# Kernel tuning notes

Measured on AMD Instinct MI355X. Metric: run time of the kernel, lower is better.

## Reference

```python
import jax, jax.numpy as jnp
import numpy as np

EMBED = 768
HEADS = 12
HEAD_DIM = EMBED // HEADS
FFN = 4 * EMBED
EPS = 1e-5


def setup_inputs() -> dict:
    key = jax.random.key(0)
    ks = jax.random.split(key, 12)
    s = 0.02
    inp = {
        'x': jax.random.normal(ks[0], (1, 4096, EMBED), dtype=jnp.float32),
        'Wq': jax.random.normal(ks[1], (EMBED, EMBED), dtype=jnp.float32) * s,
        'bq': jnp.zeros((EMBED,), jnp.float32),
        'Wk': jax.random.normal(ks[2], (EMBED, EMBED), dtype=jnp.float32) * s,
        'bk': jnp.zeros((EMBED,), jnp.float32),
        'Wv': jax.random.normal(ks[3], (EMBED, EMBED), dtype=jnp.float32) * s,
        'bv': jnp.zeros((EMBED,), jnp.float32),
        'Wo': jax.random.normal(ks[4], (EMBED, EMBED), dtype=jnp.float32) * s,
        'bo': jnp.zeros((EMBED,), jnp.float32),
        'ln1_g': jnp.ones((EMBED,), jnp.float32),
        'ln1_b': jnp.zeros((EMBED,), jnp.float32),
        'W1': jax.random.normal(ks[5], (EMBED, FFN), dtype=jnp.float32) * s,
        'b1': jnp.zeros((FFN,), jnp.float32),
        'W2': jax.random.normal(ks[6], (FFN, EMBED), dtype=jnp.float32) * s,
        'b2': jnp.zeros((EMBED,), jnp.float32),
        'ln2_g': jnp.ones((EMBED,), jnp.float32),
        'ln2_b': jnp.zeros((EMBED,), jnp.float32),
    }
    return inp


def _layernorm(x, g, b):
    mu = jnp.mean(x, axis=-1, keepdims=True)
    var = jnp.mean(jnp.square(x - mu), axis=-1, keepdims=True)
    return (x - mu) * jax.lax.rsqrt(var + EPS) * g + b


def reference(x, Wq, bq, Wk, bk, Wv, bv, Wo, bo, ln1_g, ln1_b, W1, b1, W2, b2, ln2_g, ln2_b):
    B, S, D = x.shape
    # QKV projections -> [B, H, S, d]
    def split_heads(t):
        return t.reshape(B, S, HEADS, HEAD_DIM).transpose(0, 2, 1, 3)
    q = split_heads(x @ Wq + bq)
    k = split_heads(x @ Wk + bk)
    v = split_heads(x @ Wv + bv)
    scores = jnp.einsum('bhqd,bhkd->bhqk', q, k) / np.sqrt(HEAD_DIM).astype(np.float32)
    attn = jax.nn.softmax(scores, axis=-1)
    ctx = jnp.einsum('bhqk,bhkd->bhqd', attn, v)
    ctx = ctx.transpose(0, 2, 1, 3).reshape(B, S, D)
    attn_out = ctx @ Wo + bo
    h = _layernorm(x + attn_out, ln1_g, ln1_b)
    ffn = jax.nn.gelu(h @ W1 + b1, approximate=False) @ W2 + b2
    return _layernorm(h + ffn, ln2_g, ln2_b)
```

## Files before the change

kernel.cpp:

```cpp
#include <hip/hip_runtime.h>
#include <hip/hip_bf16.h>

typedef __attribute__((ext_vector_type(8))) short s16x8;
typedef __attribute__((ext_vector_type(4))) short s16x4;
typedef __attribute__((ext_vector_type(4))) int   i32x4;
typedef __attribute__((ext_vector_type(4))) float f32x4;
typedef __attribute__((ext_vector_type(8))) __bf16 bf16x8;
typedef __attribute__((ext_vector_type(4))) __bf16 bf16x4;

__device__ __forceinline__ short f2bf(float f) {
  unsigned u = __builtin_bit_cast(unsigned, f);
  u = (u + 0x7FFFu + ((u >> 16) & 1u)) >> 16;
  return (short)u;
}
__device__ __forceinline__ float bf2f(short s) {
  unsigned u = ((unsigned)(unsigned short)s) << 16;
  return __builtin_bit_cast(float, u);
}
__device__ __forceinline__ f32x4 mfma16(s16x8 a, s16x8 b, f32x4 c) {
  return __builtin_amdgcn_mfma_f32_16x16x32_bf16(
      __builtin_bit_cast(bf16x8, a), __builtin_bit_cast(bf16x8, b), c, 0, 0, 0);
}
__device__ __forceinline__ void gload16(const void* g, void* l) {
  __builtin_amdgcn_global_load_lds(
      (const __attribute__((address_space(1))) void*)g,
      (__attribute__((address_space(3))) void*)l, 16, 0, 0);
}

__global__ __launch_bounds__(256) void prep_kernel(
    const float* __restrict__ x, short* __restrict__ xb,
    const float* __restrict__ bq, const float* __restrict__ bk,
    const float* __restrict__ bv, float* __restrict__ bqkv,
    const float* __restrict__ Wq, const float* __restrict__ Wk,
    const float* __restrict__ Wv, const float* __restrict__ Wo,
    const float* __restrict__ W1, const float* __restrict__ W2,
    short* __restrict__ wqkv_t, short* __restrict__ wo_t,
    short* __restrict__ w1_t, short* __restrict__ w2_t) {
  __shared__ float t[32][33];
  const int b = blockIdx.x, tid = threadIdx.x;
  if (b < 1536) {
    int i = b * 256 + tid;
    float4 v0 = ((const float4*)x)[i * 2];
    float4 v1 = ((const float4*)x)[i * 2 + 1];
    s16x8 o;
    o[0] = f2bf(v0.x); o[1] = f2bf(v0.y); o[2] = f2bf(v0.z); o[3] = f2bf(v0.w);
    o[4] = f2bf(v1.x); o[5] = f2bf(v1.y); o[6] = f2bf(v1.z); o[7] = f2bf(v1.w);
    *(s16x8*)&xb[i * 8] = o;
    return;
  }
  if (b < 1545) {
    int i = (b - 1536) * 256 + tid;
    if (i < 2304) bqkv[i] = i < 768 ? bq[i] : (i < 1536 ? bk[i - 768] : bv[i - 1536]);
    return;
  }
  const float* src; short* dst; int K, N, bx, by;
  if (b < 3849) {
    int t4 = b - 1545, wi = t4 / 576, r = t4 % 576;
    bx = r % 24; by = r / 24; K = 768; N = 768;
    src = wi == 0 ? Wq : wi == 1 ? Wk : wi == 2 ? Wv : Wo;
    dst = wi == 0 ? wqkv_t : wi == 1 ? wqkv_t + 768 * 768
        : wi == 2 ? wqkv_t + 2 * 768 * 768 : wo_t;
  } else if (b < 6153) {
    int r = b - 3849; bx = r % 96; by = r / 96; K = 768; N = 3072; src = W1; dst = w1_t;
  } else {
    int r = b - 6153; bx = r % 24; by = r / 24; K = 3072; N = 768; src = W2; dst = w2_t;
  }
  int n0 = bx * 32, k0 = by * 32;
  int tx = tid & 31, ty = tid >> 5;
#pragma unroll
  for (int r = 0; r < 4; ++r) t[ty + r * 8][tx] = src[(long)(k0 + ty + r * 8) * N + n0 + tx];
  __syncthreads();
#pragma unroll
  for (int r = 0; r < 4; ++r)
    dst[(long)(n0 + ty + r * 8) * K + k0 + tx] = f2bf(t[tx][ty + r * 8]);
}

template <int OUT_MODE>
__global__ __launch_bounds__(256) void gemm_kernel(const short* __restrict__ A,
                                                   const short* __restrict__ Bt,
                                                   const float* __restrict__ bias,
                                                   void* __restrict__ Cout,
                                                   short* __restrict__ vtout,
                                                   int M, int N, int Kfull, int Ksub) {
  __shared__ short As[3][64 * 64];
  __shared__ short Bs[3][64 * 64];
  const int tid = threadIdx.x;
  const int wave = tid >> 6, lane = tid & 63;
  const int lr = lane & 15, lg = lane >> 4;
  const int wm = wave >> 1, wn = wave & 1;
  const int bm = blockIdx.x, bn = blockIdx.y;
  const long koff = (long)blockIdx.z * Ksub;

  f32x4 acc[4][4] = {};

  const short* Ab = A + (long)bm * 128 * Kfull + koff;
  const short* Bb = Bt + (long)bn * 128 * Kfull + koff;

  int sj[2], sr[2], skc[2];
#pragma unroll
  for (int rnd = 0; rnd < 2; ++rnd) {
    int c = tid + rnd * 256;
    int j = c >> 3, c7 = c & 7;
    int u = c7 ^ (j & 7);
    sj[rnd] = c;
    sr[rnd] = j + ((u >> 2) << 6);
    skc[rnd] = (u & 3) * 8;
  }

  auto STAGE = [&](int buf, int k0) {
#pragma unroll
    for (int rnd = 0; rnd < 2; ++rnd) {
      gload16(Ab + (long)sr[rnd] * Kfull + k0 + skc[rnd], &As[buf][sj[rnd] * 8]);
      gload16(Bb + (long)sr[rnd] * Kfull + k0 + skc[rnd], &Bs[buf][sj[rnd] * 8]);
    }
  };
  auto COMPUTE = [&](int buf) {
    s16x8 af[4], bfr[4];
#pragma unroll
    for (int m = 0; m < 4; ++m) {
      int j = m * 16 + lr;
      int c7 = ((wm << 2) | lg) ^ (lr & 7);
      af[m] = *(const s16x8*)&As[buf][j * 64 + c7 * 8];
    }
#pragma unroll
    for (int n = 0; n < 4; ++n) {
      int j = n * 16 + lr;
      int c7 = ((wn << 2) | lg) ^ (lr & 7);
      bfr[n] = *(const s16x8*)&Bs[buf][j * 64 + c7 * 8];
    }
#pragma unroll
    for (int m = 0; m < 4; ++m)
#pragma unroll
      for (int n = 0; n < 4; ++n)
        acc[m][n] = mfma16(af[m], bfr[n], acc[m][n]);
  };

  const int nt = Ksub >> 5;
  STAGE(0, 0);
  STAGE(1, 32);
  int cur = 0;
  for (int t = 0; t < nt - 2; ++t) {
    int nb = cur + 2; if (nb >= 3) nb -= 3;
    STAGE(nb, (t + 2) * 32);
    asm volatile("s_waitcnt vmcnt(8)" ::: "memory");
    __builtin_amdgcn_s_barrier();
    __builtin_amdgcn_sched_barrier(0);
    COMPUTE(cur);
    __builtin_amdgcn_s_barrier();
    cur = (cur == 2) ? 0 : cur + 1;
  }
  asm volatile("s_waitcnt vmcnt(4)" ::: "memory");
  __builtin_amdgcn_s_barrier();
  __builtin_amdgcn_sched_barrier(0);
  COMPUTE(cur);
  __builtin_amdgcn_s_barrier();
  cur = (cur == 2) ? 0 : cur + 1;
  asm volatile("s_waitcnt vmcnt(0)" ::: "memory");
  __builtin_amdgcn_s_barrier();
  __builtin_amdgcn_sched_barrier(0);
  COMPUTE(cur);

  const int gr0 = bm * 128 + wm * 64 + lg * 4;
  const int gc0 = bn * 128 + wn * 64 + lr;
  if (OUT_MODE == 0 && vtout != nullptr && bn >= 12) {
#pragma unroll
    for (int n = 0; n < 4; ++n) {
      int col = gc0 + n * 16;
      float bb = bias[col];
#pragma unroll
      for (int m = 0; m < 4; ++m) {
        s16x4 pk;
#pragma unroll
        for (int j = 0; j < 4; ++j) pk[j] = f2bf(acc[m][n][j] + bb);
        *(s16x4*)&vtout[(long)(col - 1536) * 4096 + gr0 + m * 16] = pk;
      }
    }
    return;
  }
  float* outF = (float*)Cout + (long)blockIdx.z * M * N;
#pragma unroll
  for (int n = 0; n < 4; ++n) {
    int col = gc0 + n * 16;
    float bb = (blockIdx.z == 0) ? bias[col] : 0.f;
#pragma unroll
    for (int m = 0; m < 4; ++m) {
#pragma unroll
      for (int j = 0; j < 4; ++j) {
        int row = gr0 + m * 16 + j;
        float v = acc[m][n][j] + bb;
        if (OUT_MODE == 2) v = 0.5f * v * (1.0f + erff(v * 0.70710678118f));
        if (OUT_MODE == 1) outF[(long)row * N + col] = v;
        else ((short*)Cout)[(long)row * N + col] = f2bf(v);
      }
    }
  }
}

__global__ __launch_bounds__(256) void flash_kernel(const short* __restrict__ qkv,
                                                    const short* __restrict__ vt,
                                                    short* __restrict__ Opart,
                                                    float* __restrict__ Lpart) {
  __shared__ short Kt[2][64 * 64];
  __shared__ short Vs[2][64 * 64];
  __shared__ short Ps[128 * 72];
  const int tid = threadIdx.x;
  const int wave = tid >> 6, lane = tid & 63;
  const int lr = lane & 15, lg = lane >> 4;
  const int lb = blockIdx.x + 32 * blockIdx.y + 384 * blockIdx.z;
  const int nlb = (lb & 7) * 96 + (lb >> 3);
  const int qb = nlb & 31;
  const int h = (nlb >> 5) % 12;
  const int sp = nlb / 384;
  const int qc = h * 64;
  const int hc = 768 + h * 64;
  const int vr = h * 64;
  const float QSCALE = 0.125f * 1.44269504088896f;
  const int sbase = sp * 2048;

  auto STAGE = [&](int buf, int it) {
    const int s0 = sbase + it * 64;
#pragma unroll
    for (int i = 0; i < 2; ++i) {
      int c = tid + i * 256, row = c >> 3, ch = (c & 7) ^ (row & 7);
      gload16(&qkv[(long)(s0 + row) * 2304 + hc + ch * 8], &Kt[buf][c * 8]);
      gload16(&vt[(long)(vr + row) * 4096 + s0 + ch * 8], &Vs[buf][c * 8]);
    }
  };

  STAGE(0, 0);

#pragma unroll
  for (int i = 0; i < 4; ++i) {
    int c = tid + i * 256;
    int row = c >> 3, cq = (c & 7) * 8;
    *(i32x4*)&Ps[row * 72 + cq] =
        *(const i32x4*)&qkv[(long)(qb * 128 + row) * 2304 + qc + cq];
  }
  asm volatile("s_waitcnt vmcnt(0) lgkmcnt(0)" ::: "memory");
  __builtin_amdgcn_s_barrier();
  __builtin_amdgcn_sched_barrier(0);

  s16x8 qf[2][2];
#pragma unroll
  for (int m = 0; m < 2; ++m)
#pragma unroll
    for (int ks = 0; ks < 2; ++ks) {
      int row = wave * 32 + m * 16 + lr;
      s16x8 v = *(const s16x8*)&Ps[row * 72 + ks * 32 + lg * 8];
#pragma unroll
      for (int e = 0; e < 8; ++e) {
        __bf16 b = (__bf16)(bf2f(v[e]) * QSCALE);
        v[e] = (short)__builtin_bit_cast(unsigned short, b);
      }
      qf[m][ks] = v;
    }

  float l_part[2] = {0.f, 0.f};
  f32x4 oacc[2][4] = {};

  int cur = 0;
  for (int it = 0; it < 32; ++it) {
    if (it < 31) STAGE(cur ^ 1, it + 1);

    f32x4 sacc[2][4] = {};
#pragma unroll
    for (int ks = 0; ks < 2; ++ks) {
      s16x8 kf[4];
#pragma unroll
      for (int n = 0; n < 4; ++n) {
        int row = n * 16 + lr;
        int chk = (ks * 4 + lg) ^ (lr & 7);
        kf[n] = *(const s16x8*)&Kt[cur][row * 64 + chk * 8];
      }
      __builtin_amdgcn_s_setprio(1);
#pragma unroll
      for (int m = 0; m < 2; ++m)
#pragma unroll
        for (int n = 0; n < 4; ++n)
          sacc[m][n] = mfma16(kf[n], qf[m][ks], sacc[m][n]);
      __builtin_amdgcn_s_setprio(0);
    }
#pragma unroll
    for (int m = 0; m < 2; ++m) {
      const int prow = wave * 32 + m * 16 + lr;
      float rs = 0.f;
#pragma unroll
      for (int n = 0; n < 4; ++n) {
        float p0 = __builtin_amdgcn_exp2f(sacc[m][n][0]);
        float p1 = __builtin_amdgcn_exp2f(sacc[m][n][1]);
        float p2 = __builtin_amdgcn_exp2f(sacc[m][n][2]);
        float p3 = __builtin_amdgcn_exp2f(sacc[m][n][3]);
        rs += (p0 + p1) + (p2 + p3);
        bf16x4 pk;
        pk[0] = (__bf16)p0; pk[1] = (__bf16)p1;
        pk[2] = (__bf16)p2; pk[3] = (__bf16)p3;
        *(bf16x4*)&Ps[prow * 72 + n * 16 + lg * 4] = pk;
      }
      l_part[m] += rs;
    }
#pragma unroll
    for (int ks = 0; ks < 2; ++ks) {
      s16x8 pf[2], vf[4];
#pragma unroll
      for (int m = 0; m < 2; ++m) {
        int row = wave * 32 + m * 16 + lr;
        pf[m] = *(const s16x8*)&Ps[row * 72 + ks * 32 + lg * 8];
      }
#pragma unroll
      for (int n = 0; n < 4; ++n) {
        int row = n * 16 + lr;
        int chk = (ks * 4 + lg) ^ (lr & 7);
        vf[n] = *(const s16x8*)&Vs[cur][row * 64 + chk * 8];
      }
      __builtin_amdgcn_s_setprio(1);
#pragma unroll
      for (int m = 0; m < 2; ++m)
#pragma unroll
        for (int n = 0; n < 4; ++n)
          oacc[m][n] = mfma16(pf[m], vf[n], oacc[m][n]);
      __builtin_amdgcn_s_setprio(0);
    }
    if (it < 31) {
      asm volatile("s_waitcnt vmcnt(0)" ::: "memory");
      __builtin_amdgcn_s_barrier();
      __builtin_amdgcn_sched_barrier(0);
      cur ^= 1;
    }
  }

  const long pbase = ((long)(h * 32 + qb) * 2 + sp) * 128;
#pragma unroll
  for (int m = 0; m < 2; ++m) {
    float l = l_part[m];
    l += __shfl_xor(l, 16);
    l += __shfl_xor(l, 32);
    if (lane < 16) Lpart[pbase + wave * 32 + m * 16 + lr] = l;
  }
#pragma unroll
  for (int m = 0; m < 2; ++m)
#pragma unroll
    for (int n = 0; n < 4; ++n)
#pragma unroll
      for (int j = 0; j < 4; ++j) {
        int row = wave * 32 + m * 16 + lg * 4 + j;
        Opart[(pbase + row) * 64 + n * 16 + lr] = f2bf(oacc[m][n][j]);
      }
}

__global__ __launch_bounds__(256) void combine_kernel(const short* __restrict__ Opart,
                                                      const float* __restrict__ Lpart,
                                                      short* __restrict__ ctx) {
  const int row = blockIdx.x;
  const int col = blockIdx.y * 256 + threadIdx.x;
  const int h = col >> 6, c = col & 63;
  const int qb = row >> 7, r = row & 127;
  const long p0 = ((long)(h * 32 + qb) * 2) * 128 + r;
  const long p1 = p0 + 128;
  float l = Lpart[p0] + Lpart[p1];
  float o = bf2f(Opart[p0 * 64 + c]) + bf2f(Opart[p1 * 64 + c]);
  ctx[(long)row * 768 + col] = f2bf(o / l);
}

template <int AF, int OF>
__global__ __launch_bounds__(256) void ln_kernel(const void* __restrict__ a_,
                                                 const float* __restrict__ b,
                                                 const float* __restrict__ c,
                                                 const float* __restrict__ g,
                                                 const float* __restrict__ be,
                                                 void* __restrict__ out_) {
  const int row = blockIdx.x;
  const int tid = threadIdx.x;
  const long base = (long)row * 768;
  float v[3];
  float s1 = 0.f, s2 = 0.f;
#pragma unroll
  for (int kk = 0; kk < 3; ++kk) {
    int i = tid + kk * 256;
    float av = AF ? ((const float*)a_)[base + i] : bf2f(((const short*)a_)[base + i]);
    float x = av + b[base + i] + c[base + i];
    v[kk] = x;
    s1 += x;
    s2 += x * x;
  }
#pragma unroll
  for (int off = 1; off < 64; off <<= 1) {
    s1 += __shfl_xor(s1, off);
    s2 += __shfl_xor(s2, off);
  }
  __shared__ float ws1[4], ws2[4];
  int wave = tid >> 6;
  if ((tid & 63) == 0) { ws1[wave] = s1; ws2[wave] = s2; }
  __syncthreads();
  s1 = ws1[0] + ws1[1] + ws1[2] + ws1[3];
  s2 = ws2[0] + ws2[1] + ws2[2] + ws2[3];
  float mean = s1 * (1.f / 768.f);
  float var = s2 * (1.f / 768.f) - mean * mean;
  float rstd = rsqrtf(var + 1e-5f);
#pragma unroll
  for (int kk = 0; kk < 3; ++kk) {
    int i = tid + kk * 256;
    float o = (v[kk] - mean) * rstd * g[i] + be[i];
    if (OF) ((float*)out_)[base + i] = o;
    else    ((short*)out_)[base + i] = f2bf(o);
  }
}

extern "C" void kernel_launch(void* const* d_in, const int* in_sizes, int n_in,
                              void* d_out, int out_size, void* d_ws, size_t ws_size,
                              hipStream_t stream) {
  const float* x   = (const float*)d_in[0];
  const float* Wq  = (const float*)d_in[1];
  const float* bq  = (const float*)d_in[2];
  const float* Wk  = (const float*)d_in[3];
  const float* bk  = (const float*)d_in[4];
  const float* Wv  = (const float*)d_in[5];
  const float* bv  = (const float*)d_in[6];
  const float* Wo  = (const float*)d_in[7];
  const float* bo  = (const float*)d_in[8];
  const float* g1  = (const float*)d_in[9];
  const float* be1 = (const float*)d_in[10];
  const float* W1  = (const float*)d_in[11];
  const float* b1  = (const float*)d_in[12];
  const float* W2  = (const float*)d_in[13];
  const float* b2  = (const float*)d_in[14];
  const float* g2  = (const float*)d_in[15];
  const float* be2 = (const float*)d_in[16];

  char* ws = (char*)d_ws;
  size_t off = 0;
  auto alloc = [&](size_t bytes) {
    char* p = ws + off;
    off += (bytes + 255) & ~(size_t)255;
    return p;
  };
  short* xb     = (short*)alloc(4096ul * 768 * 2);
  short* wqkv_t = (short*)alloc(2304ul * 768 * 2);
  short* wo_t   = (short*)alloc(768ul * 768 * 2);
  short* w1_t   = (short*)alloc(3072ul * 768 * 2);
  short* w2_t   = (short*)alloc(768ul * 3072 * 2);
  float* bqkv   = (float*)alloc(2304ul * 4);
  short* qkv    = (short*)alloc(4096ul * 2304 * 2);
  short* vt     = (short*)alloc(768ul * 4096 * 2);
  short* ctx    = (short*)alloc(4096ul * 768 * 2);
  float* attn_o = (float*)alloc(4096ul * 768 * 4);
  short* h_b    = (short*)alloc(4096ul * 768 * 2);
  float* h_f    = (float*)alloc(4096ul * 768 * 4);
  short* f1     = (short*)alloc(4096ul * 3072 * 2);
  short* Opart  = (short*)f1;
  float* Lpart  = (float*)attn_o;
  float* attn_p = (float*)qkv;
  float* ffn_p  = (float*)qkv;

  prep_kernel<<<8457, 256, 0, stream>>>(x, xb, bq, bk, bv, bqkv,
                                        Wq, Wk, Wv, Wo, W1, W2,
                                        wqkv_t, wo_t, w1_t, w2_t);
  gemm_kernel<0><<<dim3(32, 18), 256, 0, stream>>>(xb, wqkv_t, bqkv, qkv, vt,
                                                   4096, 2304, 768, 768);
  flash_kernel<<<dim3(32, 12, 2), 256, 0, stream>>>(qkv, vt, Opart, Lpart);
  combine_kernel<<<dim3(4096, 3), 256, 0, stream>>>(Opart, Lpart, ctx);
  gemm_kernel<1><<<dim3(32, 6, 2), 256, 0, stream>>>(ctx, wo_t, bo, attn_p, nullptr,
                                                     4096, 768, 768, 384);
  ln_kernel<1, 0><<<4096, 256, 0, stream>>>(x, attn_p, attn_p + 4096ul * 768,
                                            g1, be1, h_b);
  gemm_kernel<2><<<dim3(32, 24), 256, 0, stream>>>(h_b, w1_t, b1, f1, nullptr,
                                                   4096, 3072, 768, 768);
  gemm_kernel<1><<<dim3(32, 6, 2), 256, 0, stream>>>(f1, w2_t, b2, ffn_p, nullptr,
                                                     4096, 768, 3072, 1536);
  ln_kernel<0, 1><<<4096, 256, 0, stream>>>(h_b, ffn_p, ffn_p + 4096ul * 768,
                                            g2, be2, (float*)d_out);
}
```

Baseline: 213.7 us.

## Use 256-row GEMM tiles with 512 threads for QKV and FFN1

Adds a BIGM template variant of the GEMM that computes 256x128 output tiles with 8 waves. The A staging and fragment indexing are reworked for a 256-row swizzled layout, and the waitcnt values are adjusted to the new count of loads per stage. This variant is used for the QKV and W1 projections, so each staged B tile is reused across twice as many rows and fewer blocks are launched. Separately, the first layernorm now reads the bf16 copy of x as its residual, saving bandwidth but adding rounding error to the residual path.

```diff
diff --git a/kernel.cpp b/kernel.cpp
--- a/kernel.cpp
+++ b/kernel.cpp
@@ -75,52 +75,67 @@
     dst[(long)(n0 + ty + r * 8) * K + k0 + tx] = f2bf(t[tx][ty + r * 8]);
 }
 
-template <int OUT_MODE>
-__global__ __launch_bounds__(256) void gemm_kernel(const short* __restrict__ A,
-                                                   const short* __restrict__ Bt,
-                                                   const float* __restrict__ bias,
-                                                   void* __restrict__ Cout,
-                                                   short* __restrict__ vtout,
-                                                   int M, int N, int Kfull, int Ksub) {
-  __shared__ short As[3][64 * 64];
+template <int OUT_MODE, int BIGM>
+__global__ __launch_bounds__(BIGM ? 512 : 256) void gemm_kernel(
+    const short* __restrict__ A, const short* __restrict__ Bt,
+    const float* __restrict__ bias, void* __restrict__ Cout,
+    short* __restrict__ vtout, int M, int N, int Kfull, int Ksub) {
+  constexpr int TM = BIGM ? 256 : 128;
+  constexpr int AJ = BIGM ? 128 : 64;
+  __shared__ short As[3][AJ * 64];
   __shared__ short Bs[3][64 * 64];
   const int tid = threadIdx.x;
   const int wave = tid >> 6, lane = tid & 63;
   const int lr = lane & 15, lg = lane >> 4;
-  const int wm = wave >> 1, wn = wave & 1;
+  const int wm = BIGM ? (wave >> 1) : (wave >> 1);
+  const int wn = wave & 1;
   const int bm = blockIdx.x, bn = blockIdx.y;
   const long koff = (long)blockIdx.z * Ksub;
 
   f32x4 acc[4][4] = {};
 
-  const short* Ab = A + (long)bm * 128 * Kfull + koff;
+  const short* Ab = A + (long)bm * TM * Kfull + koff;
   const short* Bb = Bt + (long)bn * 128 * Kfull + koff;
 
-  int sj[2], sr[2], skc[2];
-#pragma unroll
-  for (int rnd = 0; rnd < 2; ++rnd) {
-    int c = tid + rnd * 256;
-    int j = c >> 3, c7 = c & 7;
-    int u = c7 ^ (j & 7);
-    sj[rnd] = c;
-    sr[rnd] = j + ((u >> 2) << 6);
-    skc[rnd] = (u & 3) * 8;
-  }
-
   auto STAGE = [&](int buf, int k0) {
-#pragma unroll
-    for (int rnd = 0; rnd < 2; ++rnd) {
-      gload16(Ab + (long)sr[rnd] * Kfull + k0 + skc[rnd], &As[buf][sj[rnd] * 8]);
-      gload16(Bb + (long)sr[rnd] * Kfull + k0 + skc[rnd], &Bs[buf][sj[rnd] * 8]);
+    if constexpr (BIGM) {
+#pragma unroll
+      for (int rnd = 0; rnd < 2; ++rnd) {
+        int c = tid + rnd * 512;
+        int j = c >> 3, u = (c & 7) ^ (j & 7);
+        int r = j + ((u >> 2) << 7), kc = (u & 3) * 8;
+        gload16(Ab + (long)r * Kfull + k0 + kc, &As[buf][c * 8]);
+      }
+      {
+        int c = tid;
+        int j = c >> 3, u = (c & 7) ^ (j & 7);
+        int r = j + ((u >> 2) << 6), kc = (u & 3) * 8;
+        gload16(Bb + (long)r * Kfull + k0 + kc, &Bs[buf][c * 8]);
+      }
+    } else {
+#pragma unroll
+      for (int rnd = 0; rnd < 2; ++rnd) {
+        int c = tid + rnd * 256;
+        int j = c >> 3, u = (c & 7) ^ (j & 7);
+        int r = j + ((u >> 2) << 6), kc = (u & 3) * 8;
+        gload16(Ab + (long)r * Kfull + k0 + kc, &As[buf][c * 8]);
+        gload16(Bb + (long)r * Kfull + k0 + kc, &Bs[buf][c * 8]);
+      }
     }
   };
   auto COMPUTE = [&](int buf) {
     s16x8 af[4], bfr[4];
 #pragma unroll
     for (int m = 0; m < 4; ++m) {
-      int j = m * 16 + lr;
-      int c7 = ((wm << 2) | lg) ^ (lr & 7);
-      af[m] = *(const s16x8*)&As[buf][j * 64 + c7 * 8];
+      if constexpr (BIGM) {
+        int j = (wm & 1) * 64 + m * 16 + lr;
+        int c7 = (((wm >> 1) << 2) | lg) ^ (lr & 7);
+        af[m] = *(const s16x8*)&As[buf][j * 64 + c7 * 8];
+      } else {
+        int j = m * 16 + lr;
+        int c7 = ((wm << 2) | lg) ^ (lr & 7);
+        af[m] = *(const s16x8*)&As[buf][j * 64 + c7 * 8];
+      }
     }
 #pragma unroll
     for (int n = 0; n < 4; ++n) {
@@ -135,6 +150,7 @@
         acc[m][n] = mfma16(af[m], bfr[n], acc[m][n]);
   };
 
+  constexpr int LPS = BIGM ? 3 : 4;
   const int nt = Ksub >> 5;
   STAGE(0, 0);
   STAGE(1, 32);
@@ -142,14 +158,16 @@
   for (int t = 0; t < nt - 2; ++t) {
     int nb = cur + 2; if (nb >= 3) nb -= 3;
     STAGE(nb, (t + 2) * 32);
-    asm volatile("s_waitcnt vmcnt(8)" ::: "memory");
+    if constexpr (BIGM) asm volatile("s_waitcnt vmcnt(6)" ::: "memory");
+    else                asm volatile("s_waitcnt vmcnt(8)" ::: "memory");
     __builtin_amdgcn_s_barrier();
     __builtin_amdgcn_sched_barrier(0);
     COMPUTE(cur);
     __builtin_amdgcn_s_barrier();
     cur = (cur == 2) ? 0 : cur + 1;
   }
-  asm volatile("s_waitcnt vmcnt(4)" ::: "memory");
+  if constexpr (BIGM) asm volatile("s_waitcnt vmcnt(3)" ::: "memory");
+  else                asm volatile("s_waitcnt vmcnt(4)" ::: "memory");
   __builtin_amdgcn_s_barrier();
   __builtin_amdgcn_sched_barrier(0);
   COMPUTE(cur);
@@ -159,8 +177,9 @@
   __builtin_amdgcn_s_barrier();
   __builtin_amdgcn_sched_barrier(0);
   COMPUTE(cur);
-
-  const int gr0 = bm * 128 + wm * 64 + lg * 4;
+  (void)LPS;
+
+  const int gr0 = bm * TM + wm * 64 + lg * 4;
   const int gc0 = bn * 128 + wn * 64 + lr;
   if (OUT_MODE == 0 && vtout != nullptr && bn >= 12) {
 #pragma unroll
@@ -454,18 +473,18 @@
   prep_kernel<<<8457, 256, 0, stream>>>(x, xb, bq, bk, bv, bqkv,
                                         Wq, Wk, Wv, Wo, W1, W2,
                                         wqkv_t, wo_t, w1_t, w2_t);
-  gemm_kernel<0><<<dim3(32, 18), 256, 0, stream>>>(xb, wqkv_t, bqkv, qkv, vt,
-                                                   4096, 2304, 768, 768);
+  gemm_kernel<0, 1><<<dim3(16, 18), 512, 0, stream>>>(xb, wqkv_t, bqkv, qkv, vt,
+                                                      4096, 2304, 768, 768);
   flash_kernel<<<dim3(32, 12, 2), 256, 0, stream>>>(qkv, vt, Opart, Lpart);
   combine_kernel<<<dim3(4096, 3), 256, 0, stream>>>(Opart, Lpart, ctx);
-  gemm_kernel<1><<<dim3(32, 6, 2), 256, 0, stream>>>(ctx, wo_t, bo, attn_p, nullptr,
-                                                     4096, 768, 768, 384);
-  ln_kernel<1, 0><<<4096, 256, 0, stream>>>(x, attn_p, attn_p + 4096ul * 768,
+  gemm_kernel<1, 0><<<dim3(32, 6, 2), 256, 0, stream>>>(ctx, wo_t, bo, attn_p, nullptr,
+                                                        4096, 768, 768, 384);
+  ln_kernel<0, 0><<<4096, 256, 0, stream>>>(xb, attn_p, attn_p + 4096ul * 768,
                                             g1, be1, h_b);
-  gemm_kernel<2><<<dim3(32, 24), 256, 0, stream>>>(h_b, w1_t, b1, f1, nullptr,
-                                                   4096, 3072, 768, 768);
-  gemm_kernel<1><<<dim3(32, 6, 2), 256, 0, stream>>>(f1, w2_t, b2, ffn_p, nullptr,
-                                                     4096, 768, 3072, 1536);
+  gemm_kernel<2, 1><<<dim3(16, 24), 512, 0, stream>>>(h_b, w1_t, b1, f1, nullptr,
+                                                      4096, 3072, 768, 768);
+  gemm_kernel<1, 0><<<dim3(32, 6, 2), 256, 0, stream>>>(f1, w2_t, b2, ffn_p, nullptr,
+                                                        4096, 768, 3072, 1536);
   ln_kernel<0, 1><<<4096, 256, 0, stream>>>(h_b, ffn_p, ffn_p + 4096ul * 768,
                                             g2, be2, (float*)d_out);
 }
```

Measured after the change: 217.2 us. No clear change (+1.7%).
